# Optimization experiments

Hardware: AMD Instinct MI355X
Metric: run time of the kernel (lower is better)

The kernel has to match this reference:

```python
import jax, jax.numpy as jnp
import numpy as np

BN_EPS = 1e-5


def conv1x1(x, w, b):
    # x: [B,C,H,W], w: [O,C], b: [O] -> [B,O,H,W]
    return jnp.einsum('bchw,oc->bohw', x, w) + b[None, :, None, None]


def setup_inputs() -> dict:
    key = jax.random.key(0)
    ks = jax.random.split(key, 11)
    B, C, H, W = 8, 1024, 64, 32
    hid = 64  # C * rd_ratio (1/16)
    s = 0.02
    return {
        'x': jax.random.normal(ks[0], (B, C, H, W), dtype=jnp.float32),
        'theta_w': jax.random.normal(ks[1], (hid, C), dtype=jnp.float32) * s,
        'theta_b': jax.random.normal(ks[2], (hid,), dtype=jnp.float32) * s,
        'phi_w': jax.random.normal(ks[3], (hid, C), dtype=jnp.float32) * s,
        'phi_b': jax.random.normal(ks[4], (hid,), dtype=jnp.float32) * s,
        'g_w': jax.random.normal(ks[5], (hid, C), dtype=jnp.float32) * s,
        'g_b': jax.random.normal(ks[6], (hid,), dtype=jnp.float32) * s,
        'w_w': jax.random.normal(ks[7], (C, hid), dtype=jnp.float32) * s,
        'w_b': jax.random.normal(ks[8], (C,), dtype=jnp.float32) * s,
        'bn_gamma': jax.random.normal(ks[9], (C,), dtype=jnp.float32) * 0.1 + 1.0,
        'bn_beta': jax.random.normal(ks[10], (C,), dtype=jnp.float32) * 0.1,
    }


def reference(x, theta_w, theta_b, phi_w, phi_b, g_w, g_b, w_w, w_b, bn_gamma, bn_beta):
    B, C, H, W = x.shape
    hid = theta_w.shape[0]
    N = H * W
    theta = conv1x1(x, theta_w, theta_b).reshape(B, hid, N).transpose(0, 2, 1)  # [B,N,d]
    phi = conv1x1(x, phi_w, phi_b).reshape(B, hid, N)                           # [B,d,N]
    g = conv1x1(x, g_w, g_b).reshape(B, hid, N).transpose(0, 2, 1)              # [B,N,d]
    f = jnp.einsum('bnd,bdm->bnm', theta, phi) / N                              # [B,N,N]
    y = jnp.einsum('bnm,bmd->bnd', f, g)                                        # [B,N,d]
    y = y.transpose(0, 2, 1).reshape(B, hid, H, W)
    wy = conv1x1(y, w_w, w_b)                                                   # [B,C,H,W]
    # BatchNorm2d in training mode: batch statistics over (B,H,W), biased variance
    mean = wy.mean(axis=(0, 2, 3), keepdims=True)
    var = wy.var(axis=(0, 2, 3), keepdims=True)
    norm = (wy - mean) * jax.lax.rsqrt(var + BN_EPS)
    out = norm * bn_gamma[None, :, None, None] + bn_beta[None, :, None, None]
    return out + x
```

## Files before the change

### kernel.cpp

```cpp
#include <hip/hip_runtime.h>

#define B_    8
#define C_    1024
#define HID   64
#define N_    2048
#define RTOT  192

typedef __attribute__((ext_vector_type(8))) short   bf16x8;
typedef __attribute__((ext_vector_type(4))) unsigned short ush4;
typedef __attribute__((ext_vector_type(4))) float   f32x4;
typedef __attribute__((ext_vector_type(16))) float  f32x16;

#define WSB_WBF   ((size_t)0)
#define WSB_TPG   ((size_t)393216)
#define WSB_THT   ((size_t)6684672)
#define WSB_M     ((size_t)8781824)
#define WSB_G     ((size_t)8912896)
#define WSB_S     ((size_t)9043968)
#define WSB_WMBF  ((size_t)9046016)
#define WSB_SC    ((size_t)10094592)
#define WSB_SH    ((size_t)10098688)

#define MGS_FLOATS (2 * B_ * HID * HID + B_ * HID)

static __device__ __forceinline__ unsigned short f2bf(float f) {
    union { float f; unsigned u; } v; v.f = f;
    unsigned r = v.u + 0x7fffu + ((v.u >> 16) & 1u);
    return (unsigned short)(r >> 16);
}
static __device__ __forceinline__ float bf2f(unsigned short h) {
    union { unsigned u; float f; } v; v.u = ((unsigned)h) << 16;
    return v.f;
}

static __device__ __forceinline__ void gload16(const unsigned short* g, unsigned short* l) {
    __builtin_amdgcn_global_load_lds(
        (const __attribute__((address_space(1))) unsigned int*)g,
        (__attribute__((address_space(3))) unsigned int*)l, 16, 0, 0);
}

__global__ __launch_bounds__(256) void wcvt(
    const float* __restrict__ tw, const float* __restrict__ pw,
    const float* __restrict__ gw, unsigned short* __restrict__ wbf,
    float* __restrict__ mgs)
{
    int idx = blockIdx.x * 256 + threadIdx.x;
    if (blockIdx.x < 258) {
        int z = blockIdx.x * 256 + threadIdx.x;
        if (z < MGS_FLOATS) mgs[z] = 0.f;
    }
    int r = idx >> 10, k = idx & 1023;
    float v = (r < 64) ? tw[(size_t)r * 1024 + k]
            : (r < 128) ? pw[(size_t)(r - 64) * 1024 + k]
                        : gw[(size_t)(r - 128) * 1024 + k];
    wbf[idx] = f2bf(v);
}

__global__ __launch_bounds__(256, 4) void projx_mfma(
    const float* __restrict__ x, const unsigned short* __restrict__ wbf,
    const float* __restrict__ tb, const float* __restrict__ pb,
    const float* __restrict__ gb, unsigned short* __restrict__ tpgbf,
    unsigned short* __restrict__ thT)
{
    const int b = blockIdx.z, rh = blockIdx.y, n0 = blockIdx.x * 64;
    const int t = threadIdx.x, w = t >> 6, L = t & 63;
    const int wn = w & 1, wc = w >> 1;
    const int lr = L & 15, q = L >> 4;

    __shared__ unsigned short Abuf[2][64][64];
    __shared__ unsigned short Bbuf[2][96][64];

    f32x4 acc[2][3] = {};

    const int n4 = t & 15;
    const int g  = t >> 4;
    const float* xbase = x + (size_t)b * C_ * N_ + n0 + n4 * 4;

    f32x4 vr[4];
    auto loadX = [&](int s) {
        const float* p = xbase + (size_t)(64 * s + 4 * g) * N_;
#pragma unroll
        for (int j = 0; j < 4; j++)
            vr[j] = *(const f32x4*)(p + (size_t)j * N_);
    };
    auto writeA = [&](int cb) {
#pragma unroll
        for (int rrow = 0; rrow < 4; rrow++) {
            int n  = 4 * n4 + rrow;
            int sw = (n ^ (n >> 3)) & 7;
            int ss = (g >> 1) ^ sw;
            unsigned d0 = (unsigned)f2bf(vr[0][rrow]) | ((unsigned)f2bf(vr[1][rrow]) << 16);
            unsigned d1 = (unsigned)f2bf(vr[2][rrow]) | ((unsigned)f2bf(vr[3][rrow]) << 16);
            unsigned* dst = (unsigned*)&Abuf[cb][n][0] + ss * 4 + 2 * (g & 1);
            *(unsigned long long*)dst =
                (unsigned long long)d0 | ((unsigned long long)d1 << 32);
        }
    };
    auto stageB = [&](int cb, int s) {
        const int k0 = 64 * s;
#pragma unroll
        for (int i = 0; i < 3; i++) {
            int o = (i * 256 + t) * 16;
            int row = o >> 7, slot = (o >> 4) & 7, ss = slot ^ (row & 7);
            gload16(wbf + ((size_t)(96 * rh + row)) * 1024 + k0 + ss * 8,
                    &Bbuf[cb][0][0] + o / 2);
        }
    };

    const int swB = lr & 7;
    int nfa0 = wn * 32 + lr, nfa1 = wn * 32 + 16 + lr;
    const int swA0 = (nfa0 ^ (nfa0 >> 3)) & 7;
    const int swA1 = (nfa1 ^ (nfa1 >> 3)) & 7;
    auto compute = [&](int cur) {
#pragma unroll
        for (int ksub = 0; ksub < 2; ksub++) {
            bf16x8 Af[2], Bf[3];
            Af[0] = *(const bf16x8*)&Abuf[cur][nfa0][((ksub * 4 + q) ^ swA0) * 8];
            Af[1] = *(const bf16x8*)&Abuf[cur][nfa1][((ksub * 4 + q) ^ swA1) * 8];
#pragma unroll
            for (int j = 0; j < 3; j++)
                Bf[j] = *(const bf16x8*)&Bbuf[cur][wc * 48 + j * 16 + lr]
                                              [((ksub * 4 + q) ^ swB) * 8];
#pragma unroll
            for (int fa = 0; fa < 2; fa++)
#pragma unroll
                for (int j = 0; j < 3; j++)
                    acc[fa][j] = __builtin_amdgcn_mfma_f32_16x16x32_bf16(
                        Af[fa], Bf[j], acc[fa][j], 0, 0, 0);
        }
    };

    loadX(0);
    asm volatile("s_waitcnt vmcnt(0)" ::: "memory");
    writeA(0);
    stageB(0, 0);
    loadX(1);
    asm volatile("s_waitcnt vmcnt(4)" ::: "memory");
    asm volatile("s_waitcnt lgkmcnt(0)" ::: "memory");
    __builtin_amdgcn_s_barrier();

    int cur = 0;
    for (int s = 0; s < 16; s++) {
        if (s < 15) {
            writeA(cur ^ 1);
            stageB(cur ^ 1, s + 1);
        }
        if (s < 14) loadX(s + 2);
        compute(cur);
        if (s < 14)
            asm volatile("s_waitcnt vmcnt(4)" ::: "memory");
        else
            asm volatile("s_waitcnt vmcnt(0)" ::: "memory");
        asm volatile("s_waitcnt lgkmcnt(0)" ::: "memory");
        if (s < 15) __builtin_amdgcn_s_barrier();
        cur ^= 1;
    }

#pragma unroll
    for (int fa = 0; fa < 2; fa++)
#pragma unroll
        for (int j = 0; j < 3; j++) {
            int rcol = 96 * rh + 48 * wc + 16 * j + lr;
            float bias = (rcol < 64) ? tb[rcol]
                       : (rcol < 128) ? pb[rcol - 64] : gb[rcol - 128];
            ush4 o;
#pragma unroll
            for (int rr = 0; rr < 4; rr++) o[rr] = f2bf(acc[fa][j][rr] + bias);
            int nglob = n0 + wn * 32 + fa * 16 + q * 4;
            *(ush4*)(tpgbf + ((size_t)b * RTOT + rcol) * N_ + nglob) = o;
            if (rcol < HID) {
#pragma unroll
                for (int rr = 0; rr < 4; rr++)
                    thT[((size_t)b * N_ + nglob + rr) * HID + rcol] = o[rr];
            }
        }
}

__global__ __launch_bounds__(256) void gram_mfma(
    const unsigned short* __restrict__ tpgbf, float* __restrict__ Mm,
    float* __restrict__ Gg, float* __restrict__ S)
{
    const int kc = blockIdx.x, p = blockIdx.y, b = blockIdx.z;
    const int t = threadIdx.x, w = t >> 6, L = t & 63;
    const int lr = L & 15, q = L >> 4;
    const unsigned short* base = tpgbf + (size_t)b * RTOT * N_;
    const unsigned short* Arow = base + (p ? 0 : (size_t)64 * N_);
    const unsigned short* Brow = base + (p ? 0 : (size_t)128 * N_);
    const unsigned short* ap = Arow + ((size_t)(16 * w + lr)) * N_ + kc * 128 + q * 8;
    const unsigned short* bp = Brow + ((size_t)lr) * N_ + kc * 128 + q * 8;

    bf16x8 ones;
#pragma unroll
    for (int j = 0; j < 8; j++) ones[j] = (short)0x3F80;

    f32x4 acc[4] = {};
    f32x4 accs = {};
#pragma unroll
    for (int it = 0; it < 4; ++it) {
        const int kn = it * 32;
        bf16x8 a = *(const bf16x8*)(ap + kn);
#pragma unroll
        for (int g = 0; g < 4; g++) {
            bf16x8 bb = *(const bf16x8*)(bp + (size_t)g * 16 * N_ + kn);
            acc[g] = __builtin_amdgcn_mfma_f32_16x16x32_bf16(a, bb, acc[g], 0, 0, 0);
        }
        if (p) accs = __builtin_amdgcn_mfma_f32_16x16x32_bf16(a, ones, accs, 0, 0, 0);
    }
    float* outp = (p ? Gg : Mm) + (size_t)b * HID * HID;
#pragma unroll
    for (int g = 0; g < 4; g++)
#pragma unroll
        for (int r = 0; r < 4; r++) {
            int row = 16 * w + q * 4 + r, col = 16 * g + lr;
            atomicAdd(outp + row * HID + col, acc[g][r]);
        }
    if (p && lr == 0) {
#pragma unroll
        for (int r = 0; r < 4; r++)
            atomicAdd(S + b * HID + 16 * w + q * 4 + r, accs[r]);
    }
}

__global__ __launch_bounds__(512, 1) void wmstat(
    const float* __restrict__ ww, const float* __restrict__ Mm,
    const float* __restrict__ S, const float* __restrict__ G,
    const float* __restrict__ wb, const float* __restrict__ gamma,
    const float* __restrict__ beta, unsigned short* __restrict__ wmbf,
    float* __restrict__ scale, float* __restrict__ shift2)
{
    const int c0 = blockIdx.x * 4;
    const int t = threadIdx.x;
    const int b = t >> 6, lane = t & 63;

    f32x4 mrow[16], grow[16];
    {
        const f32x4* mr4 = (const f32x4*)(Mm + ((size_t)b * HID + lane) * HID);
        const f32x4* gr4 = (const f32x4*)(G  + (size_t)b * HID * HID + (size_t)lane * HID);
#pragma unroll
        for (int i = 0; i < 16; i++) mrow[i] = mr4[i];
#pragma unroll
        for (int i = 0; i < 16; i++) grow[i] = gr4[i];
    }
    const float sv = S[b * HID + lane];

    __shared__ float vsh[8][64];
    __shared__ float red[4][16];

#pragma unroll
    for (int ci = 0; ci < 4; ci++) {
        const int c = c0 + ci;
        const float wbc = wb[c];
        const float* wr = ww + (size_t)c * HID;

        float acc = 0.f;
#pragma unroll
        for (int d = 0; d < 16; d++) {
            f32x4 w4 = *(const f32x4*)(wr + 4 * d);
            acc += w4[0] * mrow[d][0] + w4[1] * mrow[d][1]
                 + w4[2] * mrow[d][2] + w4[3] * mrow[d][3];
        }
        unsigned short us = f2bf(acc * (1.0f / N_));
        wmbf[((size_t)b * C_ + c) * HID + lane] = us;
        float v = bf2f(us);
        float t1 = v * sv;
        for (int off = 32; off; off >>= 1) t1 += __shfl_down(t1, off);
        t1 = __shfl(t1, 0);

        __syncthreads();
        vsh[b][lane] = v;
        __syncthreads();

        const f32x4* vb4 = (const f32x4*)&vsh[b][0];
        float inner = 0.f;
#pragma unroll
        for (int fo = 0; fo < 16; fo++) {
            f32x4 vv = vb4[fo];
            inner = fmaf(grow[fo][0], vv[0], inner);
            inner = fmaf(grow[fo][1], vv[1], inner);
            inner = fmaf(grow[fo][2], vv[2], inner);
            inner = fmaf(grow[fo][3], vv[3], inner);
        }
        float qq = v * inner;
        for (int off = 32; off; off >>= 1) qq += __shfl_down(qq, off);
        qq = __shfl(qq, 0);

        if (lane == 0) {
            red[ci][b] = t1;
            red[ci][8 + b] = qq + 2.f * wbc * t1;
        }
    }
    __syncthreads();
    if (t < 4) {
        const int c = c0 + t;
        float asum = 0.f, asq = 0.f;
#pragma unroll
        for (int i = 0; i < 8; i++) { asum += red[t][i]; asq += red[t][8 + i]; }
        const float wbc = wb[c];
        const float cnt = (float)B_ * (float)N_;
        const float inv = 1.0f / cnt;
        float mean = (asum + cnt * wbc) * inv;
        float e2   = (asq + cnt * wbc * wbc) * inv;
        float var  = e2 - mean * mean;
        float sc   = gamma[c] * rsqrtf(var + 1e-5f);
        scale[c]  = sc;
        shift2[c] = beta[c] - mean * sc + sc * wbc;
    }
}

__global__ __launch_bounds__(256) void finalk_mfma(
    const unsigned short* __restrict__ wmbf, const unsigned short* __restrict__ thT,
    const float* __restrict__ x, const float* __restrict__ scale,
    const float* __restrict__ shift2, float* __restrict__ out)
{
    const int b = blockIdx.z, c0 = blockIdx.y * 32, n0b = blockIdx.x * 128;
    const int t = threadIdx.x, w = t >> 6, L = t & 63;
    const int n0 = n0b + w * 32;
    const int rr = L & 31, kh = L >> 5;

    const unsigned short* apw = wmbf + ((size_t)b * C_ + c0 + rr) * HID + kh * 8;
    const unsigned short* bpt = thT + ((size_t)b * N_ + n0 + rr) * HID + kh * 8;

    float xv[16];
#pragma unroll
    for (int r = 0; r < 16; r++) {
        int cl = (r & 3) + 8 * (r >> 2) + 4 * kh;
        xv[r] = x[((size_t)b * C_ + c0 + cl) * N_ + n0 + rr];
    }

    f32x16 acc = {};
#pragma unroll
    for (int kk = 0; kk < 4; kk++) {
        bf16x8 A  = *(const bf16x8*)(apw + kk * 16);
        bf16x8 Bv = *(const bf16x8*)(bpt + kk * 16);
        acc = __builtin_amdgcn_mfma_f32_32x32x16_bf16(A, Bv, acc, 0, 0, 0);
    }

#pragma unroll
    for (int r = 0; r < 16; r++) {
        int cl = (r & 3) + 8 * (r >> 2) + 4 * kh;
        int c  = c0 + cl;
        size_t off = ((size_t)b * C_ + c) * N_ + n0 + rr;
        out[off] = fmaf(scale[c], acc[r], shift2[c]) + xv[r];
    }
}

extern "C" void kernel_launch(void* const* d_in, const int* in_sizes, int n_in,
                              void* d_out, int out_size, void* d_ws, size_t ws_size,
                              hipStream_t stream)
{
    const float* x  = (const float*)d_in[0];
    const float* tw = (const float*)d_in[1];
    const float* tb = (const float*)d_in[2];
    const float* pw = (const float*)d_in[3];
    const float* pb = (const float*)d_in[4];
    const float* gw = (const float*)d_in[5];
    const float* gb = (const float*)d_in[6];
    const float* ww = (const float*)d_in[7];
    const float* wb = (const float*)d_in[8];
    const float* gamma = (const float*)d_in[9];
    const float* beta  = (const float*)d_in[10];
    float* out = (float*)d_out;

    char* ws = (char*)d_ws;
    unsigned short* wbf   = (unsigned short*)(ws + WSB_WBF);
    unsigned short* tpgbf = (unsigned short*)(ws + WSB_TPG);
    unsigned short* thT   = (unsigned short*)(ws + WSB_THT);
    float* Mm   = (float*)(ws + WSB_M);
    float* Gg   = (float*)(ws + WSB_G);
    float* S    = (float*)(ws + WSB_S);
    unsigned short* wmbf = (unsigned short*)(ws + WSB_WMBF);
    float* scl  = (float*)(ws + WSB_SC);
    float* shf  = (float*)(ws + WSB_SH);

    wcvt<<<dim3(RTOT * 1024 / 256), 256, 0, stream>>>(tw, pw, gw, wbf, Mm);
    projx_mfma<<<dim3(32, 2, B_), 256, 0, stream>>>(x, wbf, tb, pb, gb, tpgbf, thT);
    gram_mfma<<<dim3(16, 2, B_), 256, 0, stream>>>(tpgbf, Mm, Gg, S);
    wmstat<<<C_ / 4, 512, 0, stream>>>(ww, Mm, S, Gg, wb, gamma, beta, wmbf, scl, shf);
    finalk_mfma<<<dim3(16, 32, B_), 256, 0, stream>>>(wmbf, thT, x, scl, shf, out);
}
```

Baseline: 196.0 us.

## Retile projection GEMM so each block computes all 192 outputs for 32 positions

The projection kernel used to split the 192 output rows across two blocks, so each 64-position tile of x was read from global memory twice. Now each block covers all 192 rows for a 32-column strip, so x is read once, while the weight tile staged per k-step doubles and the grid becomes 64x8. This removes the duplicate reads of the large fp32 input. In exchange, shared memory per block grows, the occupancy hint drops from 4 to 2, and each block issues smaller A-tile writes.

After: 193.2 us, median of 2. Within noise of the previous version (-1.4%).

```diff
diff --git a/kernel.cpp b/kernel.cpp
--- a/kernel.cpp
+++ b/kernel.cpp
@@ -56,77 +56,69 @@
     wbf[idx] = f2bf(v);
 }
 
-__global__ __launch_bounds__(256, 4) void projx_mfma(
+__global__ __launch_bounds__(256, 2) void projx_mfma(
     const float* __restrict__ x, const unsigned short* __restrict__ wbf,
     const float* __restrict__ tb, const float* __restrict__ pb,
     const float* __restrict__ gb, unsigned short* __restrict__ tpgbf,
     unsigned short* __restrict__ thT)
 {
-    const int b = blockIdx.z, rh = blockIdx.y, n0 = blockIdx.x * 64;
+    const int b = blockIdx.y, n0 = blockIdx.x * 32;
     const int t = threadIdx.x, w = t >> 6, L = t & 63;
     const int wn = w & 1, wc = w >> 1;
     const int lr = L & 15, q = L >> 4;
 
-    __shared__ unsigned short Abuf[2][64][64];
-    __shared__ unsigned short Bbuf[2][96][64];
-
-    f32x4 acc[2][3] = {};
-
-    const int n4 = t & 15;
-    const int g  = t >> 4;
+    __shared__ unsigned short Abuf[2][32][64];
+    __shared__ unsigned short Bbuf[2][192][64];
+
+    f32x4 acc[6] = {};
+
+    const int n4 = t & 7;
+    const int g  = t >> 3;
     const float* xbase = x + (size_t)b * C_ * N_ + n0 + n4 * 4;
 
-    f32x4 vr[4];
+    f32x4 vr[2];
     auto loadX = [&](int s) {
-        const float* p = xbase + (size_t)(64 * s + 4 * g) * N_;
-#pragma unroll
-        for (int j = 0; j < 4; j++)
-            vr[j] = *(const f32x4*)(p + (size_t)j * N_);
+        const float* p = xbase + (size_t)(64 * s + 2 * g) * N_;
+        vr[0] = *(const f32x4*)(p);
+        vr[1] = *(const f32x4*)(p + N_);
     };
     auto writeA = [&](int cb) {
 #pragma unroll
         for (int rrow = 0; rrow < 4; rrow++) {
             int n  = 4 * n4 + rrow;
             int sw = (n ^ (n >> 3)) & 7;
-            int ss = (g >> 1) ^ sw;
-            unsigned d0 = (unsigned)f2bf(vr[0][rrow]) | ((unsigned)f2bf(vr[1][rrow]) << 16);
-            unsigned d1 = (unsigned)f2bf(vr[2][rrow]) | ((unsigned)f2bf(vr[3][rrow]) << 16);
-            unsigned* dst = (unsigned*)&Abuf[cb][n][0] + ss * 4 + 2 * (g & 1);
-            *(unsigned long long*)dst =
-                (unsigned long long)d0 | ((unsigned long long)d1 << 32);
+            int ss = (g >> 2) ^ sw;
+            unsigned val = (unsigned)f2bf(vr[0][rrow]) | ((unsigned)f2bf(vr[1][rrow]) << 16);
+            ((unsigned*)&Abuf[cb][n][0])[ss * 4 + (g & 3)] = val;
         }
     };
     auto stageB = [&](int cb, int s) {
         const int k0 = 64 * s;
 #pragma unroll
-        for (int i = 0; i < 3; i++) {
+        for (int i = 0; i < 6; i++) {
             int o = (i * 256 + t) * 16;
             int row = o >> 7, slot = (o >> 4) & 7, ss = slot ^ (row & 7);
-            gload16(wbf + ((size_t)(96 * rh + row)) * 1024 + k0 + ss * 8,
+            gload16(wbf + ((size_t)row) * 1024 + k0 + ss * 8,
                     &Bbuf[cb][0][0] + o / 2);
         }
     };
 
     const int swB = lr & 7;
-    int nfa0 = wn * 32 + lr, nfa1 = wn * 32 + 16 + lr;
-    const int swA0 = (nfa0 ^ (nfa0 >> 3)) & 7;
-    const int swA1 = (nfa1 ^ (nfa1 >> 3)) & 7;
+    const int nfa = wn * 16 + lr;
+    const int swA = (nfa ^ (nfa >> 3)) & 7;
     auto compute = [&](int cur) {
 #pragma unroll
         for (int ksub = 0; ksub < 2; ksub++) {
-            bf16x8 Af[2], Bf[3];
-            Af[0] = *(const bf16x8*)&Abuf[cur][nfa0][((ksub * 4 + q) ^ swA0) * 8];
-            Af[1] = *(const bf16x8*)&Abuf[cur][nfa1][((ksub * 4 + q) ^ swA1) * 8];
-#pragma unroll
-            for (int j = 0; j < 3; j++)
-                Bf[j] = *(const bf16x8*)&Bbuf[cur][wc * 48 + j * 16 + lr]
+            bf16x8 Af = *(const bf16x8*)&Abuf[cur][nfa][((ksub * 4 + q) ^ swA) * 8];
+            bf16x8 Bf[6];
+#pragma unroll
+            for (int j = 0; j < 6; j++)
+                Bf[j] = *(const bf16x8*)&Bbuf[cur][wc * 96 + j * 16 + lr]
                                               [((ksub * 4 + q) ^ swB) * 8];
 #pragma unroll
-            for (int fa = 0; fa < 2; fa++)
-#pragma unroll
-                for (int j = 0; j < 3; j++)
-                    acc[fa][j] = __builtin_amdgcn_mfma_f32_16x16x32_bf16(
-                        Af[fa], Bf[j], acc[fa][j], 0, 0, 0);
+            for (int j = 0; j < 6; j++)
+                acc[j] = __builtin_amdgcn_mfma_f32_16x16x32_bf16(
+                    Af, Bf[j], acc[j], 0, 0, 0);
         }
     };
 
@@ -135,7 +127,7 @@
     writeA(0);
     stageB(0, 0);
     loadX(1);
-    asm volatile("s_waitcnt vmcnt(4)" ::: "memory");
+    asm volatile("s_waitcnt vmcnt(2)" ::: "memory");
     asm volatile("s_waitcnt lgkmcnt(0)" ::: "memory");
     __builtin_amdgcn_s_barrier();
 
@@ -148,7 +140,7 @@
         if (s < 14) loadX(s + 2);
         compute(cur);
         if (s < 14)
-            asm volatile("s_waitcnt vmcnt(4)" ::: "memory");
+            asm volatile("s_waitcnt vmcnt(2)" ::: "memory");
         else
             asm volatile("s_waitcnt vmcnt(0)" ::: "memory");
         asm volatile("s_waitcnt lgkmcnt(0)" ::: "memory");
@@ -157,23 +149,21 @@
     }
 
 #pragma unroll
-    for (int fa = 0; fa < 2; fa++)
-#pragma unroll
-        for (int j = 0; j < 3; j++) {
-            int rcol = 96 * rh + 48 * wc + 16 * j + lr;
-            float bias = (rcol < 64) ? tb[rcol]
-                       : (rcol < 128) ? pb[rcol - 64] : gb[rcol - 128];
-            ush4 o;
-#pragma unroll
-            for (int rr = 0; rr < 4; rr++) o[rr] = f2bf(acc[fa][j][rr] + bias);
-            int nglob = n0 + wn * 32 + fa * 16 + q * 4;
-            *(ush4*)(tpgbf + ((size_t)b * RTOT + rcol) * N_ + nglob) = o;
-            if (rcol < HID) {
-#pragma unroll
-                for (int rr = 0; rr < 4; rr++)
-                    thT[((size_t)b * N_ + nglob + rr) * HID + rcol] = o[rr];
-            }
-        }
+    for (int j = 0; j < 6; j++) {
+        int rcol = 96 * wc + 16 * j + lr;
+        float bias = (rcol < 64) ? tb[rcol]
+                   : (rcol < 128) ? pb[rcol - 64] : gb[rcol - 128];
+        ush4 o;
+#pragma unroll
+        for (int rr = 0; rr < 4; rr++) o[rr] = f2bf(acc[j][rr] + bias);
+        int nglob = n0 + wn * 16 + q * 4;
+        *(ush4*)(tpgbf + ((size_t)b * RTOT + rcol) * N_ + nglob) = o;
+        if (rcol < HID) {
+#pragma unroll
+            for (int rr = 0; rr < 4; rr++)
+                thT[((size_t)b * N_ + nglob + rr) * HID + rcol] = o[rr];
+        }
+    }
 }
 
 __global__ __launch_bounds__(256) void gram_mfma(
@@ -373,7 +363,7 @@
     float* shf  = (float*)(ws + WSB_SH);
 
     wcvt<<<dim3(RTOT * 1024 / 256), 256, 0, stream>>>(tw, pw, gw, wbf, Mm);
-    projx_mfma<<<dim3(32, 2, B_), 256, 0, stream>>>(x, wbf, tb, pb, gb, tpgbf, thT);
+    projx_mfma<<<dim3(64, B_), 256, 0, stream>>>(x, wbf, tb, pb, gb, tpgbf, thT);
     gram_mfma<<<dim3(16, 2, B_), 256, 0, stream>>>(tpgbf, Mm, Gg, S);
     wmstat<<<C_ / 4, 512, 0, stream>>>(ww, Mm, S, Gg, wb, gamma, beta, wmbf, scl, shf);
     finalk_mfma<<<dim3(16, 32, B_), 256, 0, stream>>>(wmbf, thT, x, scl, shf, out);
```
